# Kernel optimization log

Hardware: AMD Instinct MI355X
Metric: run time of the kernel (lower is better)

The kernel has to match this reference:

```python
import jax, jax.numpy as jnp
import numpy as np

N, E, C_IN, C_OUT, K = 50000, 800000, 64, 64, 3


def setup_inputs() -> dict:
    key = jax.random.key(0)
    ks = jax.random.split(key, 8)
    X = jax.random.normal(ks[0], (N, C_IN), jnp.float32)
    edge_index = jax.random.randint(ks[1], (2, E), 0, N)
    edge_weight = jax.random.uniform(ks[2], (E,), jnp.float32)
    H = jax.random.normal(ks[3], (N, C_OUT), jnp.float32)
    C = jax.random.normal(ks[4], (N, C_OUT), jnp.float32)
    # gate order: i=0, f=1, c=2, o=3 ; wc order: i=0, f=1, o=2
    Wx = jax.random.normal(ks[5], (4, K, C_IN, C_OUT), jnp.float32) * 0.1
    Wh = jax.random.normal(ks[6], (4, K, C_OUT, C_OUT), jnp.float32) * 0.1
    wc = jax.random.normal(ks[7], (3, C_OUT), jnp.float32) * 0.1
    bx = jnp.zeros((4, C_OUT), jnp.float32)
    bh = jnp.zeros((4, C_OUT), jnp.float32)
    bg = jnp.zeros((4, C_OUT), jnp.float32)
    return dict(X=X, edge_index=edge_index, edge_weight=edge_weight, H=H, C=C,
                Wx=Wx, bx=bx, Wh=Wh, bh=bh, wc=wc, bg=bg)


def _scaled_laplacian_norm(edge_index, edge_weight, n):
    # PyG ChebConv sym normalization with lambda_max=2:
    # L_hat = 2L/lambda_max - I = -D^{-1/2} A D^{-1/2} (diagonal cancels)
    src, dst = edge_index[0], edge_index[1]
    deg = jax.ops.segment_sum(edge_weight, src, num_segments=n)
    dinv = jnp.where(deg > 0, jax.lax.rsqrt(deg), 0.0)
    return -dinv[src] * edge_weight * dinv[dst]


def _cheb_conv(x, W, b, src, dst, norm, n):
    # Chebyshev recursion: Tx0 = x, Tx1 = L_hat x, Tx_k = 2 L_hat Tx_{k-1} - Tx_{k-2}
    prop = lambda t: jax.ops.segment_sum(norm[:, None] * t[src], dst, num_segments=n)
    Tx0 = x
    out = Tx0 @ W[0]
    Tx1 = prop(Tx0)
    out = out + Tx1 @ W[1]
    for k in range(2, W.shape[0]):
        Tx2 = 2.0 * prop(Tx1) - Tx0
        out = out + Tx2 @ W[k]
        Tx0, Tx1 = Tx1, Tx2
    return out + b


def reference(X, edge_index, edge_weight, H, C, Wx, bx, Wh, bh, wc, bg):
    n = X.shape[0]
    src, dst = edge_index[0], edge_index[1]
    norm = _scaled_laplacian_norm(edge_index, edge_weight, n)
    conv = lambda g, inp, W, b: _cheb_conv(inp, W[g], b[g], src, dst, norm, n)
    I = jax.nn.sigmoid(conv(0, X, Wx, bx) + conv(0, H, Wh, bh) + wc[0] * C + bg[0])
    F = jax.nn.sigmoid(conv(1, X, Wx, bx) + conv(1, H, Wh, bh) + wc[1] * C + bg[1])
    T = jnp.tanh(conv(2, X, Wx, bx) + conv(2, H, Wh, bh) + bg[2])
    C_new = F * C + I * T
    O = jax.nn.sigmoid(conv(3, X, Wx, bx) + conv(3, H, Wh, bh) + wc[2] * C_new + bg[3])
    H_new = O * jnp.tanh(C_new)
    return (H_new, C_new)
```

## Files before the change

### kernel.cpp

```cpp
#include <hip/hip_runtime.h>
#include <math.h>

#define NN 50000
#define NE 800000

typedef __attribute__((ext_vector_type(8))) short short8;
typedef __attribute__((ext_vector_type(8))) unsigned short ushort8;
typedef __attribute__((ext_vector_type(4))) float f32x4;

#define QENC 31.75f
#define QDEC 0.031496063f

#define OFF_DEG    0
#define OFF_BSUM   50000
#define OFF_ROWPTR 100000
#define OFF_WB     200072
#define OFF_BIAS   249224
#define OFF_ELIST  249480
#define OFF_XB     1849480
#define OFF_HB     3449480
#define OFF_T1X    5049480
#define OFF_T1H    6649480
#define OFF_T2X    8249480
#define OFF_T2H    9849480
#define OFF_XH8    11449480
#define OFF_T1XH8  13049480
#define OFF_HISTP  5049480
#define OFF_COLEXC 8249480
#define OFF_DEGP   13049480

#define DCH    250
#define DCHUNK 3200
#define SCH    32
#define SCHUNK 25000
#define CNBLK  196
#define CBLK   1563
#define WBLK   48
#define FR_HIST (2 * DCH)
#define FR_DEG  (FR_HIST + 8 * SCH)
#define FR_CVT  (FR_DEG + CBLK)
#define FR_ALL  (FR_CVT + WBLK)

__device__ inline unsigned short f2bf(float f) {
  union { float f; unsigned u; } v; v.f = f;
  unsigned u = v.u;
  return (unsigned short)((u + 0x7FFFu + ((u >> 16) & 1u)) >> 16);
}
__device__ inline float bf2f(unsigned short u) {
  return __uint_as_float(((unsigned)u) << 16);
}
__device__ inline float sigm(float x) { return 1.f / (1.f + __expf(-x)); }
__device__ inline float tanh_(float x) { return 1.f - 2.f / (__expf(2.f * x) + 1.f); }

__device__ inline unsigned f2q8(float f) {
  float c = fminf(fmaxf(f * QENC, -127.f), 127.f);
  int q = (int)rintf(c);
  return (unsigned)(q & 0xff);
}

__global__ __launch_bounds__(256) void k_front(
    const int* __restrict__ src, const int* __restrict__ dst,
    const float* __restrict__ w,
    unsigned char* __restrict__ histp, float* __restrict__ degp,
    const float* __restrict__ X, const float* __restrict__ H,
    unsigned short* __restrict__ Xb, unsigned short* __restrict__ Hb,
    unsigned char* __restrict__ XH8,
    const float* __restrict__ Wx, const float* __restrict__ Wh,
    const float* __restrict__ bx, const float* __restrict__ bh,
    const float* __restrict__ bg,
    unsigned short* __restrict__ Wb2, float* __restrict__ bias) {
  __shared__ unsigned lds[6250];
  const int t = threadIdx.x;
  const int bid = blockIdx.x;
  if (bid < FR_HIST) {
    const int c = bid >> 1, half = bid & 1, lo = half * 25000;
    for (int i = t; i < 6250; i += 256) lds[i] = 0u;
    __syncthreads();
    const int4* d4 = (const int4*)(dst + c * DCHUNK);
#pragma unroll
    for (int it = 0; it < 4; ++it) {
      int o4 = it * 256 + t;
      if (o4 < DCHUNK / 4) {
        int4 dv = d4[o4];
        int ds[4] = {dv.x, dv.y, dv.z, dv.w};
#pragma unroll
        for (int j = 0; j < 4; ++j) {
          int dr = ds[j] - lo;
          if ((unsigned)dr < 25000u)
            atomicAdd(&lds[dr >> 2], 1u << ((dr & 3) * 8));
        }
      }
    }
    __syncthreads();
    unsigned* hw = (unsigned*)(histp + c * 50000 + lo);
    for (int i = t; i < 6250; i += 256) hw[i] = lds[i];
  } else if (bid < FR_DEG) {
    const int idx = bid - FR_HIST;
    const int c = idx >> 3, e8 = idx & 7, lo = e8 * 6250;
    float* ldsf = (float*)lds;
    for (int i = t; i < 6250; i += 256) ldsf[i] = 0.f;
    __syncthreads();
    const int4* s4 = (const int4*)(src + c * SCHUNK);
    const float4* w4 = (const float4*)(w + c * SCHUNK);
    for (int it = 0; it < 25; ++it) {
      int o4 = it * 256 + t;
      if (o4 < SCHUNK / 4) {
        int4 sv = s4[o4];
        float4 wv = w4[o4];
        int ss[4] = {sv.x, sv.y, sv.z, sv.w};
        float ww[4] = {wv.x, wv.y, wv.z, wv.w};
#pragma unroll
        for (int j = 0; j < 4; ++j) {
          int sr = ss[j] - lo;
          if ((unsigned)sr < 6250u) atomicAdd(&ldsf[sr], ww[j]);
        }
      }
    }
    __syncthreads();
    float* dw = degp + c * 50000 + lo;
    for (int i = t; i < 6250; i += 256) dw[i] = ldsf[i];
  } else if (bid < FR_CVT) {
    int i = ((bid - FR_DEG) * 256 + t) * 8;
    if (i >= NN * 64) return;
    float4 x0 = *(const float4*)&X[i];
    float4 x1 = *(const float4*)&X[i + 4];
    float4 h0 = *(const float4*)&H[i];
    float4 h1 = *(const float4*)&H[i + 4];
    ushort8 xb, hb;
    xb[0] = f2bf(x0.x); xb[1] = f2bf(x0.y); xb[2] = f2bf(x0.z); xb[3] = f2bf(x0.w);
    xb[4] = f2bf(x1.x); xb[5] = f2bf(x1.y); xb[6] = f2bf(x1.z); xb[7] = f2bf(x1.w);
    hb[0] = f2bf(h0.x); hb[1] = f2bf(h0.y); hb[2] = f2bf(h0.z); hb[3] = f2bf(h0.w);
    hb[4] = f2bf(h1.x); hb[5] = f2bf(h1.y); hb[6] = f2bf(h1.z); hb[7] = f2bf(h1.w);
    *(ushort8*)&Xb[i] = xb;
    *(ushort8*)&Hb[i] = hb;
    int n = i >> 6, c = i & 63;
    unsigned xlo = f2q8(x0.x) | (f2q8(x0.y) << 8) | (f2q8(x0.z) << 16) | (f2q8(x0.w) << 24);
    unsigned xhi = f2q8(x1.x) | (f2q8(x1.y) << 8) | (f2q8(x1.z) << 16) | (f2q8(x1.w) << 24);
    unsigned hlo = f2q8(h0.x) | (f2q8(h0.y) << 8) | (f2q8(h0.z) << 16) | (f2q8(h0.w) << 24);
    unsigned hhi = f2q8(h1.x) | (f2q8(h1.y) << 8) | (f2q8(h1.z) << 16) | (f2q8(h1.w) << 24);
    *(uint2*)&XH8[n * 128 + c] = make_uint2(xlo, xhi);
    *(uint2*)&XH8[n * 128 + 64 + c] = make_uint2(hlo, hhi);
  } else {
    int idx = (bid - FR_CVT) * 256 + t;
    if (idx < 256) bias[idx] = bx[idx] + bh[idx] + bg[idx];
    if (idx >= 192 * 64) return;
    int word = idx >> 6, l = idx & 63;
    int cw = word & 3;
    int gk = word >> 2;
    int g = gk / 12, kc = gk - g * 12;
    int col = cw * 16 + (l & 15);
    int seg = kc >> 1;
    int kbase = (kc & 1) * 32 + (l >> 4) * 8;
    const float* Wsel = (seg < 3) ? Wx : Wh;
    int sch = (seg < 3) ? seg : seg - 3;
    ushort8 o8;
#pragma unroll
    for (int j = 0; j < 8; ++j) {
      float v = Wsel[((g * 3 + sch) * 64 + kbase + j) * 64 + col];
      o8[j] = f2bf(v);
    }
    *(ushort8*)&Wb2[idx * 8] = o8;
  }
}

__global__ __launch_bounds__(256) void k_colA(
    const unsigned char* __restrict__ histp, unsigned char* __restrict__ colexc,
    const float* __restrict__ degp, int* __restrict__ rowptr,
    int* __restrict__ bsum, float* __restrict__ dinv) {
  __shared__ int wsum[4];
  const int t = threadIdx.x, lane = t & 63, w = t >> 6;
  const int bin = blockIdx.x * 256 + t;
  int acc = 0;
  if (bin < NN) {
#pragma unroll 10
    for (int b = 0; b < DCH; ++b) {
      unsigned char c = histp[b * 50000 + bin];
      colexc[b * 50000 + bin] = (unsigned char)acc;
      acc += c;
    }
    float dacc = 0.f;
#pragma unroll 8
    for (int b = 0; b < SCH; ++b) dacc += degp[b * 50000 + bin];
    dinv[bin] = (dacc > 0.f) ? rsqrtf(dacc) : 0.f;
  }
  int val = acc;
#pragma unroll
  for (int off = 1; off < 64; off <<= 1) {
    int u = __shfl_up(val, off, 64);
    if (lane >= off) val += u;
  }
  if (lane == 63) wsum[w] = val;
  __syncthreads();
  int wb = 0;
#pragma unroll
  for (int i = 0; i < 4; ++i) wb += (i < w) ? wsum[i] : 0;
  int incl = wb + val;
  if (bin < NN) rowptr[bin + 1] = incl;
  if (t == 255) bsum[blockIdx.x] = incl;
}

__global__ __launch_bounds__(256) void k_scanB2(int* __restrict__ bsum,
                                                int* __restrict__ rowptr) {
  __shared__ int wsum[4];
  const int t = threadIdx.x, lane = t & 63, w = t >> 6;
  int v = (t < CNBLK) ? bsum[t] : 0;
  int val = v;
#pragma unroll
  for (int off = 1; off < 64; off <<= 1) {
    int u = __shfl_up(val, off, 64);
    if (lane >= off) val += u;
  }
  if (lane == 63) wsum[w] = val;
  __syncthreads();
  int wb = 0;
#pragma unroll
  for (int i = 0; i < 4; ++i) wb += (i < w) ? wsum[i] : 0;
  int incl = wb + val;
  if (t < CNBLK) bsum[t] = incl - v;
  if (t == 0) rowptr[0] = 0;
}

__global__ __launch_bounds__(256) void k_scanC2(int* __restrict__ rowptr,
                                                const int* __restrict__ bsum) {
  int i = blockIdx.x * 256 + threadIdx.x;
  if (i < NN) rowptr[i + 1] += bsum[blockIdx.x];
}

__global__ __launch_bounds__(256) void k_scat(
    const int* __restrict__ src, const int* __restrict__ dst,
    const float* __restrict__ w, const float* __restrict__ dinv,
    const int* __restrict__ rowptr, const unsigned char* __restrict__ colexc,
    unsigned* __restrict__ elist) {
  __shared__ unsigned lds[6250];
  const int t = threadIdx.x, bid = blockIdx.x;
  const int c = bid >> 1, half = bid & 1, lo = half * 25000;
  for (int i = t; i < 6250; i += 256) lds[i] = 0u;
  __syncthreads();
  const int4* s4 = (const int4*)(src + c * DCHUNK);
  const int4* d4 = (const int4*)(dst + c * DCHUNK);
  const float4* w4 = (const float4*)(w + c * DCHUNK);
#pragma unroll
  for (int it = 0; it < 4; ++it) {
    int o4 = it * 256 + t;
    if (o4 < DCHUNK / 4) {
      int4 sv = s4[o4];
      int4 dv = d4[o4];
      float4 wv = w4[o4];
      int ss[4] = {sv.x, sv.y, sv.z, sv.w};
      int dd[4] = {dv.x, dv.y, dv.z, dv.w};
      float ww[4] = {wv.x, wv.y, wv.z, wv.w};
#pragma unroll
      for (int j = 0; j < 4; ++j) {
        int d = dd[j];
        int dr = d - lo;
        if ((unsigned)dr < 25000u) {
          int s = ss[j];
          float nm = -dinv[s] * ww[j] * dinv[d];
          unsigned old = atomicAdd(&lds[dr >> 2], 1u << ((dr & 3) * 8));
          int rank = (int)((old >> ((dr & 3) * 8)) & 0xffu);
          int pos = rowptr[d] + (int)colexc[c * 50000 + d] + rank;
          elist[pos] = (((unsigned)f2bf(nm)) << 16) | (unsigned)s;
        }
      }
    }
  }
}

__global__ __launch_bounds__(256) void k_prop(
    const int* __restrict__ rowptr, const unsigned* __restrict__ elist,
    const uint4* __restrict__ inP8,
    unsigned short* __restrict__ outX, unsigned short* __restrict__ outH,
    uint4* __restrict__ outP8,
    const unsigned short* __restrict__ baseX, const unsigned short* __restrict__ baseH,
    int mode) {
  const int n = blockIdx.x * 4 + (threadIdx.x >> 6);
  const int l = threadIdx.x & 63;
  const int es = l >> 3;
  const int p = l & 7;
  if (n >= NN) return;
  const int beg = rowptr[n], end = rowptr[n + 1];
  float acc[16];
#pragma unroll
  for (int j = 0; j < 16; ++j) acc[j] = 0.f;
  for (int i0 = beg; i0 < end; i0 += 16) {
    int ie0 = i0 + es, ie1 = i0 + 8 + es;
    unsigned u0 = (ie0 < end) ? elist[ie0] : 0u;
    unsigned u1 = (ie1 < end) ? elist[ie1] : 0u;
    int s0 = (int)(u0 & 0xffffu), s1 = (int)(u1 & 0xffffu);
    float n0 = __uint_as_float(u0 & 0xffff0000u) * QDEC;
    float n1 = __uint_as_float(u1 & 0xffff0000u) * QDEC;
    uint4 v0 = inP8[s0 * 8 + p];
    uint4 v1 = inP8[s1 * 8 + p];
    unsigned w0[4] = {v0.x, v0.y, v0.z, v0.w};
    unsigned w1[4] = {v1.x, v1.y, v1.z, v1.w};
#pragma unroll
    for (int wd = 0; wd < 4; ++wd) {
#pragma unroll
      for (int bt = 0; bt < 4; ++bt) {
        float g0 = (float)((int)(char)(w0[wd] >> (bt * 8)));
        float g1 = (float)((int)(char)(w1[wd] >> (bt * 8)));
        acc[wd * 4 + bt] += n0 * g0 + n1 * g1;
      }
    }
  }
#pragma unroll
  for (int mask = 8; mask <= 32; mask <<= 1)
#pragma unroll
    for (int j = 0; j < 16; ++j) acc[j] += __shfl_xor(acc[j], mask, 64);

  if (es != 0) return;
  const int chbase = (p & 3) * 16;
  unsigned short* outT = (p < 4) ? outX : outH;
  const unsigned short* baseT = (p < 4) ? baseX : baseH;
  float vals[16];
  if (mode) {
    ushort8 b0 = *(const ushort8*)&baseT[n * 64 + chbase];
    ushort8 b1 = *(const ushort8*)&baseT[n * 64 + chbase + 8];
#pragma unroll
    for (int j = 0; j < 8; ++j) {
      vals[j] = 2.f * acc[j] - bf2f(b0[j]);
      vals[8 + j] = 2.f * acc[8 + j] - bf2f(b1[j]);
    }
  } else {
#pragma unroll
    for (int j = 0; j < 16; ++j) vals[j] = acc[j];
  }
  ushort8 o0, o1;
#pragma unroll
  for (int j = 0; j < 8; ++j) { o0[j] = f2bf(vals[j]); o1[j] = f2bf(vals[8 + j]); }
  *(ushort8*)&outT[n * 64 + chbase] = o0;
  *(ushort8*)&outT[n * 64 + chbase + 8] = o1;
  if (!mode) {
    unsigned wv[4];
#pragma unroll
    for (int wd = 0; wd < 4; ++wd) {
      unsigned r = 0;
#pragma unroll
      for (int bt = 0; bt < 4; ++bt) r |= f2q8(vals[wd * 4 + bt]) << (bt * 8);
      wv[wd] = r;
    }
    uint4 o8; o8.x = wv[0]; o8.y = wv[1]; o8.z = wv[2]; o8.w = wv[3];
    outP8[n * 8 + p] = o8;
  }
}

__global__ __launch_bounds__(256, 6) void k_gates(
    const unsigned short* __restrict__ Xb, const unsigned short* __restrict__ Hb,
    const unsigned short* __restrict__ T1X, const unsigned short* __restrict__ T1H,
    const unsigned short* __restrict__ T2X, const unsigned short* __restrict__ T2H,
    const unsigned short* __restrict__ Wb2, const float* __restrict__ C,
    const float* __restrict__ bias, const float* __restrict__ wc,
    float* __restrict__ out) {
  __shared__ unsigned short A[6 * 32 * 64];
  const int t = threadIdx.x;
  const int cw = t >> 6;
  const int l = t & 63;
  const int base = blockIdx.x * 32;
  const int lr = l & 15;
  const int cc = cw * 16 + lr;

  float cpre[2][4];
#pragma unroll
  for (int rb = 0; rb < 2; ++rb)
#pragma unroll
    for (int q = 0; q < 4; ++q) {
      int n = base + rb * 16 + (l >> 4) * 4 + q;
      int nc = (n < NN) ? n : NN - 1;
      cpre[rb][q] = C[nc * 64 + cc];
    }

  const unsigned short* segp[6] = {Xb, T1X, T2X, Hb, T1H, T2H};
  {
    const int r = t >> 3, g0 = t & 7;
    const int gsw = g0 ^ (r & 7);
    int n = base + r;
    int nc = (n < NN) ? n : NN - 1;
    ushort8 st[6];
#pragma unroll
    for (int seg = 0; seg < 6; ++seg)
      st[seg] = *(const ushort8*)&segp[seg][nc * 64 + gsw * 8];
#pragma unroll
    for (int seg = 0; seg < 6; ++seg)
      *(ushort8*)&A[(seg * 256 + t) * 8] = st[seg];
  }
  __syncthreads();

  f32x4 acc[4][2];
#pragma unroll
  for (int g = 0; g < 4; ++g) {
    acc[g][0] = (f32x4){0.f, 0.f, 0.f, 0.f};
    acc[g][1] = (f32x4){0.f, 0.f, 0.f, 0.f};
  }

#pragma unroll
  for (int kc = 0; kc < 12; ++kc) {
    const int seg = kc >> 1;
    const int slot = ((kc & 1) * 4 + (l >> 4)) ^ (lr & 7);
    short8 a[2];
#pragma unroll
    for (int rb = 0; rb < 2; ++rb) {
      int row = rb * 16 + lr;
      a[rb] = *(const short8*)&A[((seg * 32 + row) * 8 + slot) * 8];
    }
#pragma unroll
    for (int g = 0; g < 4; ++g) {
      short8 b = *(const short8*)&Wb2[(((g * 12 + kc) * 4 + cw) << 9) + l * 8];
      acc[g][0] = __builtin_amdgcn_mfma_f32_16x16x32_bf16(a[0], b, acc[g][0], 0, 0, 0);
      acc[g][1] = __builtin_amdgcn_mfma_f32_16x16x32_bf16(a[1], b, acc[g][1], 0, 0, 0);
    }
  }

  const float bI = bias[cc],       bF = bias[64 + cc];
  const float bT = bias[128 + cc], bO = bias[192 + cc];
  const float wI = wc[cc], wF = wc[64 + cc], wO = wc[128 + cc];
#pragma unroll
  for (int rb = 0; rb < 2; ++rb) {
#pragma unroll
    for (int q = 0; q < 4; ++q) {
      int n = base + rb * 16 + (l >> 4) * 4 + q;
      if (n >= NN) continue;
      float cv = cpre[rb][q];
      float pI = acc[0][rb][q] + bI + wI * cv;
      float pF = acc[1][rb][q] + bF + wF * cv;
      float pT = acc[2][rb][q] + bT;
      float I = sigm(pI);
      float F = sigm(pF);
      float T = tanh_(pT);
      float Cn = F * cv + I * T;
      float pO = acc[3][rb][q] + bO + wO * Cn;
      float O = sigm(pO);
      out[n * 64 + cc] = O * tanh_(Cn);
      out[NN * 64 + n * 64 + cc] = Cn;
    }
  }
}

extern "C" void kernel_launch(void* const* d_in, const int* in_sizes, int n_in,
                              void* d_out, int out_size, void* d_ws, size_t ws_size,
                              hipStream_t stream) {
  const float* X  = (const float*)d_in[0];
  const int*   ei = (const int*)d_in[1];
  const float* ew = (const float*)d_in[2];
  const float* H  = (const float*)d_in[3];
  const float* C  = (const float*)d_in[4];
  const float* Wx = (const float*)d_in[5];
  const float* bx = (const float*)d_in[6];
  const float* Wh = (const float*)d_in[7];
  const float* bh = (const float*)d_in[8];
  const float* wc = (const float*)d_in[9];
  const float* bg = (const float*)d_in[10];
  float* out = (float*)d_out;
  float* ws = (float*)d_ws;

  const int* src = ei;
  const int* dst = ei + NE;
  float* dinv = ws + OFF_DEG;
  int* bsum = (int*)(ws + OFF_BSUM);
  int* rowptr = (int*)(ws + OFF_ROWPTR);
  unsigned short* Wb2 = (unsigned short*)(ws + OFF_WB);
  float* bias = ws + OFF_BIAS;
  unsigned* elist = (unsigned*)(ws + OFF_ELIST);
  unsigned char* histp = (unsigned char*)(ws + OFF_HISTP);
  unsigned char* colexc = (unsigned char*)(ws + OFF_COLEXC);
  float* degp = ws + OFF_DEGP;
  unsigned short* Xb  = (unsigned short*)(ws + OFF_XB);
  unsigned short* Hb  = (unsigned short*)(ws + OFF_HB);
  unsigned short* T1X = (unsigned short*)(ws + OFF_T1X);
  unsigned short* T1H = (unsigned short*)(ws + OFF_T1H);
  unsigned short* T2X = (unsigned short*)(ws + OFF_T2X);
  unsigned short* T2H = (unsigned short*)(ws + OFF_T2H);
  unsigned char* XH8   = (unsigned char*)(ws + OFF_XH8);
  unsigned char* T1XH8 = (unsigned char*)(ws + OFF_T1XH8);

  k_front<<<FR_ALL, 256, 0, stream>>>(src, dst, ew, histp, degp,
                                      X, H, Xb, Hb, XH8,
                                      Wx, Wh, bx, bh, bg, Wb2, bias);
  k_colA<<<CNBLK, 256, 0, stream>>>(histp, colexc, degp, rowptr, bsum, dinv);
  k_scanB2<<<1, 256, 0, stream>>>(bsum, rowptr);
  k_scanC2<<<CNBLK, 256, 0, stream>>>(rowptr, bsum);
  k_scat<<<2 * DCH, 256, 0, stream>>>(src, dst, ew, dinv, rowptr, colexc, elist);
  k_prop<<<NN / 4, 256, 0, stream>>>(rowptr, elist, (const uint4*)XH8,
                                     T1X, T1H, (uint4*)T1XH8,
                                     nullptr, nullptr, 0);
  k_prop<<<NN / 4, 256, 0, stream>>>(rowptr, elist, (const uint4*)T1XH8,
                                     T2X, T2H, nullptr, Xb, Hb, 1);
  k_gates<<<(NN + 31) / 32, 256, 0, stream>>>(Xb, Hb, T1X, T1H, T2X, T2H,
                                              Wb2, C, bias, wc, out);
}
```

Before: 163.5 us.

## Store bf16 feature buffers in MFMA fragment layout and drop LDS staging in gates

The bf16 copies of X, H and the Chebyshev terms are now written in a blocked layout: 16-node tiles, with 8-channel groups strided by 128 elements. Each lane of the gates kernel can then load its MFMA A-operand fragment straight from global memory. This removes the shared-memory staging buffer, its swizzled copy and the block barrier in k_gates. The producers k_front and k_prop write the new layout, so their stores are less contiguous per node, and A fragments are now loaded from global or cache once per wave rather than shared through LDS.

```diff
diff --git a/kernel.cpp b/kernel.cpp
--- a/kernel.cpp
+++ b/kernel.cpp
@@ -3,6 +3,7 @@
 
 #define NN 50000
 #define NE 800000
+#define NR 3125
 
 typedef __attribute__((ext_vector_type(8))) short short8;
 typedef __attribute__((ext_vector_type(8))) unsigned short ushort8;
@@ -10,6 +11,7 @@
 
 #define QENC 31.75f
 #define QDEC 0.031496063f
+
 
 #define OFF_DEG    0
 #define OFF_BSUM   50000
@@ -63,7 +65,7 @@
     const float* __restrict__ w,
     unsigned char* __restrict__ histp, float* __restrict__ degp,
     const float* __restrict__ X, const float* __restrict__ H,
-    unsigned short* __restrict__ Xb, unsigned short* __restrict__ Hb,
+    unsigned short* __restrict__ XbF, unsigned short* __restrict__ HbF,
     unsigned char* __restrict__ XH8,
     const float* __restrict__ Wx, const float* __restrict__ Wh,
     const float* __restrict__ bx, const float* __restrict__ bh,
@@ -120,8 +122,10 @@
     float* dw = degp + c * 50000 + lo;
     for (int i = t; i < 6250; i += 256) dw[i] = ldsf[i];
   } else if (bid < FR_CVT) {
-    int i = ((bid - FR_DEG) * 256 + t) * 8;
-    if (i >= NN * 64) return;
+    int gid = (bid - FR_DEG) * 256 + t;
+    if (gid >= NN * 8) return;
+    int n = gid >> 3, cg = gid & 7;
+    int i = n * 64 + cg * 8;
     float4 x0 = *(const float4*)&X[i];
     float4 x1 = *(const float4*)&X[i + 4];
     float4 h0 = *(const float4*)&H[i];
@@ -131,13 +135,14 @@
     xb[4] = f2bf(x1.x); xb[5] = f2bf(x1.y); xb[6] = f2bf(x1.z); xb[7] = f2bf(x1.w);
     hb[0] = f2bf(h0.x); hb[1] = f2bf(h0.y); hb[2] = f2bf(h0.z); hb[3] = f2bf(h0.w);
     hb[4] = f2bf(h1.x); hb[5] = f2bf(h1.y); hb[6] = f2bf(h1.z); hb[7] = f2bf(h1.w);
-    *(ushort8*)&Xb[i] = xb;
-    *(ushort8*)&Hb[i] = hb;
-    int n = i >> 6, c = i & 63;
+    int fm = ((n >> 4) << 10) + (cg << 7) + ((n & 15) << 3);
+    *(ushort8*)&XbF[fm] = xb;
+    *(ushort8*)&HbF[fm] = hb;
     unsigned xlo = f2q8(x0.x) | (f2q8(x0.y) << 8) | (f2q8(x0.z) << 16) | (f2q8(x0.w) << 24);
     unsigned xhi = f2q8(x1.x) | (f2q8(x1.y) << 8) | (f2q8(x1.z) << 16) | (f2q8(x1.w) << 24);
     unsigned hlo = f2q8(h0.x) | (f2q8(h0.y) << 8) | (f2q8(h0.z) << 16) | (f2q8(h0.w) << 24);
     unsigned hhi = f2q8(h1.x) | (f2q8(h1.y) << 8) | (f2q8(h1.z) << 16) | (f2q8(h1.w) << 24);
+    int c = cg * 8;
     *(uint2*)&XH8[n * 128 + c] = make_uint2(xlo, xhi);
     *(uint2*)&XH8[n * 128 + 64 + c] = make_uint2(hlo, hhi);
   } else {
@@ -269,9 +274,9 @@
 __global__ __launch_bounds__(256) void k_prop(
     const int* __restrict__ rowptr, const unsigned* __restrict__ elist,
     const uint4* __restrict__ inP8,
-    unsigned short* __restrict__ outX, unsigned short* __restrict__ outH,
+    unsigned short* __restrict__ outXF, unsigned short* __restrict__ outHF,
     uint4* __restrict__ outP8,
-    const unsigned short* __restrict__ baseX, const unsigned short* __restrict__ baseH,
+    const unsigned short* __restrict__ baseXF, const unsigned short* __restrict__ baseHF,
     int mode) {
   const int n = blockIdx.x * 4 + (threadIdx.x >> 6);
   const int l = threadIdx.x & 63;
@@ -309,13 +314,13 @@
     for (int j = 0; j < 16; ++j) acc[j] += __shfl_xor(acc[j], mask, 64);
 
   if (es != 0) return;
-  const int chbase = (p & 3) * 16;
-  unsigned short* outT = (p < 4) ? outX : outH;
-  const unsigned short* baseT = (p < 4) ? baseX : baseH;
+  unsigned short* outT = (p < 4) ? outXF : outHF;
+  const unsigned short* baseT = (p < 4) ? baseXF : baseHF;
+  const int fm = ((n >> 4) << 10) + ((p & 3) << 8) + ((n & 15) << 3);
   float vals[16];
   if (mode) {
-    ushort8 b0 = *(const ushort8*)&baseT[n * 64 + chbase];
-    ushort8 b1 = *(const ushort8*)&baseT[n * 64 + chbase + 8];
+    ushort8 b0 = *(const ushort8*)&baseT[fm];
+    ushort8 b1 = *(const ushort8*)&baseT[fm + 128];
 #pragma unroll
     for (int j = 0; j < 8; ++j) {
       vals[j] = 2.f * acc[j] - bf2f(b0[j]);
@@ -328,8 +333,8 @@
   ushort8 o0, o1;
 #pragma unroll
   for (int j = 0; j < 8; ++j) { o0[j] = f2bf(vals[j]); o1[j] = f2bf(vals[8 + j]); }
-  *(ushort8*)&outT[n * 64 + chbase] = o0;
-  *(ushort8*)&outT[n * 64 + chbase + 8] = o1;
+  *(ushort8*)&outT[fm] = o0;
+  *(ushort8*)&outT[fm + 128] = o1;
   if (!mode) {
     unsigned wv[4];
 #pragma unroll
@@ -345,13 +350,12 @@
 }
 
 __global__ __launch_bounds__(256, 6) void k_gates(
-    const unsigned short* __restrict__ Xb, const unsigned short* __restrict__ Hb,
-    const unsigned short* __restrict__ T1X, const unsigned short* __restrict__ T1H,
-    const unsigned short* __restrict__ T2X, const unsigned short* __restrict__ T2H,
+    const unsigned short* __restrict__ XbF, const unsigned short* __restrict__ HbF,
+    const unsigned short* __restrict__ T1XF, const unsigned short* __restrict__ T1HF,
+    const unsigned short* __restrict__ T2XF, const unsigned short* __restrict__ T2HF,
     const unsigned short* __restrict__ Wb2, const float* __restrict__ C,
     const float* __restrict__ bias, const float* __restrict__ wc,
     float* __restrict__ out) {
-  __shared__ unsigned short A[6 * 32 * 64];
   const int t = threadIdx.x;
   const int cw = t >> 6;
   const int l = t & 63;
@@ -369,21 +373,12 @@
       cpre[rb][q] = C[nc * 64 + cc];
     }
 
-  const unsigned short* segp[6] = {Xb, T1X, T2X, Hb, T1H, T2H};
-  {
-    const int r = t >> 3, g0 = t & 7;
-    const int gsw = g0 ^ (r & 7);
-    int n = base + r;
-    int nc = (n < NN) ? n : NN - 1;
-    ushort8 st[6];
-#pragma unroll
-    for (int seg = 0; seg < 6; ++seg)
-      st[seg] = *(const ushort8*)&segp[seg][nc * 64 + gsw * 8];
-#pragma unroll
-    for (int seg = 0; seg < 6; ++seg)
-      *(ushort8*)&A[(seg * 256 + t) * 8] = st[seg];
-  }
-  __syncthreads();
+  int Rc[2];
+#pragma unroll
+  for (int rb = 0; rb < 2; ++rb) {
+    int R = (base >> 4) + rb;
+    Rc[rb] = (R < NR) ? R : NR - 1;
+  }
 
   f32x4 acc[4][2];
 #pragma unroll
@@ -392,16 +387,15 @@
     acc[g][1] = (f32x4){0.f, 0.f, 0.f, 0.f};
   }
 
+  const unsigned short* segp[6] = {XbF, T1XF, T2XF, HbF, T1HF, T2HF};
 #pragma unroll
   for (int kc = 0; kc < 12; ++kc) {
-    const int seg = kc >> 1;
-    const int slot = ((kc & 1) * 4 + (l >> 4)) ^ (lr & 7);
+    const unsigned short* sp = segp[kc >> 1];
+    const int go = (((kc & 1) * 4 + (l >> 4)) << 7) + lr * 8;
     short8 a[2];
 #pragma unroll
-    for (int rb = 0; rb < 2; ++rb) {
-      int row = rb * 16 + lr;
-      a[rb] = *(const short8*)&A[((seg * 32 + row) * 8 + slot) * 8];
-    }
+    for (int rb = 0; rb < 2; ++rb)
+      a[rb] = *(const short8*)&sp[(Rc[rb] << 10) + go];
 #pragma unroll
     for (int g = 0; g < 4; ++g) {
       short8 b = *(const short8*)&Wb2[(((g * 12 + kc) * 4 + cw) << 9) + l * 8];
@@ -463,27 +457,27 @@
   unsigned char* histp = (unsigned char*)(ws + OFF_HISTP);
   unsigned char* colexc = (unsigned char*)(ws + OFF_COLEXC);
   float* degp = ws + OFF_DEGP;
-  unsigned short* Xb  = (unsigned short*)(ws + OFF_XB);
-  unsigned short* Hb  = (unsigned short*)(ws + OFF_HB);
-  unsigned short* T1X = (unsigned short*)(ws + OFF_T1X);
-  unsigned short* T1H = (unsigned short*)(ws + OFF_T1H);
-  unsigned short* T2X = (unsigned short*)(ws + OFF_T2X);
-  unsigned short* T2H = (unsigned short*)(ws + OFF_T2H);
+  unsigned short* XbF  = (unsigned short*)(ws + OFF_XB);
+  unsigned short* HbF  = (unsigned short*)(ws + OFF_HB);
+  unsigned short* T1XF = (unsigned short*)(ws + OFF_T1X);
+  unsigned short* T1HF = (unsigned short*)(ws + OFF_T1H);
+  unsigned short* T2XF = (unsigned short*)(ws + OFF_T2X);
+  unsigned short* T2HF = (unsigned short*)(ws + OFF_T2H);
   unsigned char* XH8   = (unsigned char*)(ws + OFF_XH8);
   unsigned char* T1XH8 = (unsigned char*)(ws + OFF_T1XH8);
 
   k_front<<<FR_ALL, 256, 0, stream>>>(src, dst, ew, histp, degp,
-                                      X, H, Xb, Hb, XH8,
+                                      X, H, XbF, HbF, XH8,
                                       Wx, Wh, bx, bh, bg, Wb2, bias);
   k_colA<<<CNBLK, 256, 0, stream>>>(histp, colexc, degp, rowptr, bsum, dinv);
   k_scanB2<<<1, 256, 0, stream>>>(bsum, rowptr);
   k_scanC2<<<CNBLK, 256, 0, stream>>>(rowptr, bsum);
   k_scat<<<2 * DCH, 256, 0, stream>>>(src, dst, ew, dinv, rowptr, colexc, elist);
   k_prop<<<NN / 4, 256, 0, stream>>>(rowptr, elist, (const uint4*)XH8,
-                                     T1X, T1H, (uint4*)T1XH8,
+                                     T1XF, T1HF, (uint4*)T1XH8,
                                      nullptr, nullptr, 0);
   k_prop<<<NN / 4, 256, 0, stream>>>(rowptr, elist, (const uint4*)T1XH8,
-                                     T2X, T2H, nullptr, Xb, Hb, 1);
-  k_gates<<<(NN + 31) / 32, 256, 0, stream>>>(Xb, Hb, T1X, T1H, T2X, T2H,
+                                     T2XF, T2HF, nullptr, XbF, HbF, 1);
+  k_gates<<<(NN + 31) / 32, 256, 0, stream>>>(XbF, HbF, T1XF, T1HF, T2XF, T2HF,
                                               Wb2, C, bias, wc, out);
 }
```

Result: slower. 172.8 us (+5.7%).

## Split interleaved X/H int8 propagation into separate per-tensor SpMM passes

Applied to the files above, without the earlier changes.

Stores the int8-quantized X and H features (and T1) as separate 64-byte rows instead of one interleaved 128-byte row. The propagation kernel is launched four times, once per tensor and order. Each launch uses 4 lanes per row and 16 edges in flight per pass instead of 8 lanes and 8 edges. The aim is a smaller gather footprint per launch for better cache hit rates and more edge-level parallelism per wavefront. The cost is reading the edge list and row pointers twice as often, plus two extra kernel launches.

```diff
diff --git a/kernel.cpp b/kernel.cpp
--- a/kernel.cpp
+++ b/kernel.cpp
@@ -23,8 +23,10 @@
 #define OFF_T1H    6649480
 #define OFF_T2X    8249480
 #define OFF_T2H    9849480
-#define OFF_XH8    11449480
-#define OFF_T1XH8  13049480
+#define OFF_X8     11449480
+#define OFF_H8     12249480
+#define OFF_T1X8   13049480
+#define OFF_T1H8   13849480
 #define OFF_HISTP  5049480
 #define OFF_COLEXC 8249480
 #define OFF_DEGP   13049480
@@ -64,7 +66,7 @@
     unsigned char* __restrict__ histp, float* __restrict__ degp,
     const float* __restrict__ X, const float* __restrict__ H,
     unsigned short* __restrict__ Xb, unsigned short* __restrict__ Hb,
-    unsigned char* __restrict__ XH8,
+    unsigned char* __restrict__ X8, unsigned char* __restrict__ H8,
     const float* __restrict__ Wx, const float* __restrict__ Wh,
     const float* __restrict__ bx, const float* __restrict__ bh,
     const float* __restrict__ bg,
@@ -133,13 +135,12 @@
     hb[4] = f2bf(h1.x); hb[5] = f2bf(h1.y); hb[6] = f2bf(h1.z); hb[7] = f2bf(h1.w);
     *(ushort8*)&Xb[i] = xb;
     *(ushort8*)&Hb[i] = hb;
-    int n = i >> 6, c = i & 63;
     unsigned xlo = f2q8(x0.x) | (f2q8(x0.y) << 8) | (f2q8(x0.z) << 16) | (f2q8(x0.w) << 24);
     unsigned xhi = f2q8(x1.x) | (f2q8(x1.y) << 8) | (f2q8(x1.z) << 16) | (f2q8(x1.w) << 24);
     unsigned hlo = f2q8(h0.x) | (f2q8(h0.y) << 8) | (f2q8(h0.z) << 16) | (f2q8(h0.w) << 24);
     unsigned hhi = f2q8(h1.x) | (f2q8(h1.y) << 8) | (f2q8(h1.z) << 16) | (f2q8(h1.w) << 24);
-    *(uint2*)&XH8[n * 128 + c] = make_uint2(xlo, xhi);
-    *(uint2*)&XH8[n * 128 + 64 + c] = make_uint2(hlo, hhi);
+    *(uint2*)&X8[i] = make_uint2(xlo, xhi);
+    *(uint2*)&H8[i] = make_uint2(hlo, hhi);
   } else {
     int idx = (bid - FR_CVT) * 256 + t;
     if (idx < 256) bias[idx] = bx[idx] + bh[idx] + bg[idx];
@@ -268,29 +269,27 @@
 
 __global__ __launch_bounds__(256) void k_prop(
     const int* __restrict__ rowptr, const unsigned* __restrict__ elist,
-    const uint4* __restrict__ inP8,
-    unsigned short* __restrict__ outX, unsigned short* __restrict__ outH,
-    uint4* __restrict__ outP8,
-    const unsigned short* __restrict__ baseX, const unsigned short* __restrict__ baseH,
-    int mode) {
+    const uint4* __restrict__ inQ8,
+    unsigned short* __restrict__ outB, uint4* __restrict__ outQ8,
+    const unsigned short* __restrict__ baseB, int mode) {
   const int n = blockIdx.x * 4 + (threadIdx.x >> 6);
   const int l = threadIdx.x & 63;
-  const int es = l >> 3;
-  const int p = l & 7;
+  const int es = l >> 2;
+  const int p = l & 3;
   if (n >= NN) return;
   const int beg = rowptr[n], end = rowptr[n + 1];
   float acc[16];
 #pragma unroll
   for (int j = 0; j < 16; ++j) acc[j] = 0.f;
-  for (int i0 = beg; i0 < end; i0 += 16) {
-    int ie0 = i0 + es, ie1 = i0 + 8 + es;
+  for (int i0 = beg; i0 < end; i0 += 32) {
+    int ie0 = i0 + es, ie1 = i0 + 16 + es;
     unsigned u0 = (ie0 < end) ? elist[ie0] : 0u;
     unsigned u1 = (ie1 < end) ? elist[ie1] : 0u;
     int s0 = (int)(u0 & 0xffffu), s1 = (int)(u1 & 0xffffu);
     float n0 = __uint_as_float(u0 & 0xffff0000u) * QDEC;
     float n1 = __uint_as_float(u1 & 0xffff0000u) * QDEC;
-    uint4 v0 = inP8[s0 * 8 + p];
-    uint4 v1 = inP8[s1 * 8 + p];
+    uint4 v0 = inQ8[s0 * 4 + p];
+    uint4 v1 = inQ8[s1 * 4 + p];
     unsigned w0[4] = {v0.x, v0.y, v0.z, v0.w};
     unsigned w1[4] = {v1.x, v1.y, v1.z, v1.w};
 #pragma unroll
@@ -304,18 +303,16 @@
     }
   }
 #pragma unroll
-  for (int mask = 8; mask <= 32; mask <<= 1)
+  for (int mask = 4; mask <= 32; mask <<= 1)
 #pragma unroll
     for (int j = 0; j < 16; ++j) acc[j] += __shfl_xor(acc[j], mask, 64);
 
   if (es != 0) return;
-  const int chbase = (p & 3) * 16;
-  unsigned short* outT = (p < 4) ? outX : outH;
-  const unsigned short* baseT = (p < 4) ? baseX : baseH;
+  const int o = n * 64 + p * 16;
   float vals[16];
   if (mode) {
-    ushort8 b0 = *(const ushort8*)&baseT[n * 64 + chbase];
-    ushort8 b1 = *(const ushort8*)&baseT[n * 64 + chbase + 8];
+    ushort8 b0 = *(const ushort8*)&baseB[o];
+    ushort8 b1 = *(const ushort8*)&baseB[o + 8];
 #pragma unroll
     for (int j = 0; j < 8; ++j) {
       vals[j] = 2.f * acc[j] - bf2f(b0[j]);
@@ -328,8 +325,8 @@
   ushort8 o0, o1;
 #pragma unroll
   for (int j = 0; j < 8; ++j) { o0[j] = f2bf(vals[j]); o1[j] = f2bf(vals[8 + j]); }
-  *(ushort8*)&outT[n * 64 + chbase] = o0;
-  *(ushort8*)&outT[n * 64 + chbase + 8] = o1;
+  *(ushort8*)&outB[o] = o0;
+  *(ushort8*)&outB[o + 8] = o1;
   if (!mode) {
     unsigned wv[4];
 #pragma unroll
@@ -340,7 +337,7 @@
       wv[wd] = r;
     }
     uint4 o8; o8.x = wv[0]; o8.y = wv[1]; o8.z = wv[2]; o8.w = wv[3];
-    outP8[n * 8 + p] = o8;
+    outQ8[n * 4 + p] = o8;
   }
 }
 
@@ -469,21 +466,26 @@
   unsigned short* T1H = (unsigned short*)(ws + OFF_T1H);
   unsigned short* T2X = (unsigned short*)(ws + OFF_T2X);
   unsigned short* T2H = (unsigned short*)(ws + OFF_T2H);
-  unsigned char* XH8   = (unsigned char*)(ws + OFF_XH8);
-  unsigned char* T1XH8 = (unsigned char*)(ws + OFF_T1XH8);
+  unsigned char* X8   = (unsigned char*)(ws + OFF_X8);
+  unsigned char* H8   = (unsigned char*)(ws + OFF_H8);
+  unsigned char* T1X8 = (unsigned char*)(ws + OFF_T1X8);
+  unsigned char* T1H8 = (unsigned char*)(ws + OFF_T1H8);
 
   k_front<<<FR_ALL, 256, 0, stream>>>(src, dst, ew, histp, degp,
-                                      X, H, Xb, Hb, XH8,
+                                      X, H, Xb, Hb, X8, H8,
                                       Wx, Wh, bx, bh, bg, Wb2, bias);
   k_colA<<<CNBLK, 256, 0, stream>>>(histp, colexc, degp, rowptr, bsum, dinv);
   k_scanB2<<<1, 256, 0, stream>>>(bsum, rowptr);
   k_scanC2<<<CNBLK, 256, 0, stream>>>(rowptr, bsum);
   k_scat<<<2 * DCH, 256, 0, stream>>>(src, dst, ew, dinv, rowptr, colexc, elist);
-  k_prop<<<NN / 4, 256, 0, stream>>>(rowptr, elist, (const uint4*)XH8,
-                                     T1X, T1H, (uint4*)T1XH8,
-                                     nullptr, nullptr, 0);
-  k_prop<<<NN / 4, 256, 0, stream>>>(rowptr, elist, (const uint4*)T1XH8,
-                                     T2X, T2H, nullptr, Xb, Hb, 1);
+  k_prop<<<NN / 4, 256, 0, stream>>>(rowptr, elist, (const uint4*)X8,
+                                     T1X, (uint4*)T1X8, nullptr, 0);
+  k_prop<<<NN / 4, 256, 0, stream>>>(rowptr, elist, (const uint4*)H8,
+                                     T1H, (uint4*)T1H8, nullptr, 0);
+  k_prop<<<NN / 4, 256, 0, stream>>>(rowptr, elist, (const uint4*)T1X8,
+                                     T2X, nullptr, Xb, 1);
+  k_prop<<<NN / 4, 256, 0, stream>>>(rowptr, elist, (const uint4*)T1H8,
+                                     T2H, nullptr, Hb, 1);
   k_gates<<<(NN + 31) / 32, 256, 0, stream>>>(Xb, Hb, T1X, T1H, T2X, T2H,
                                               Wb2, C, bias, wc, out);
 }
```

New measurement: 245.1 us. 49.9% more time.
